# Optimization experiments

Hardware: AMD Instinct MI355X
Metric: run time of the kernel (lower is better)

Reference implementation:

```python
import jax, jax.numpy as jnp
import numpy as np

PROPAGATION_RANGE = 2
PROP_OUT = PROPAGATION_RANGE - 1  # propagation_out_range


def setup_inputs() -> dict:
    key = jax.random.key(0)
    k1, k2 = jax.random.split(key)
    B, D, H, W = 2, 48, 512, 640
    neighbors = 9
    depth_min = jnp.full((B,), 425.0, dtype=jnp.float32)
    depth_max = jnp.full((B,), 935.0, dtype=jnp.float32)
    # depth samples uniformly inside [depth_min, depth_max]
    u = jax.random.uniform(k1, (B, D, H, W), dtype=jnp.float32)
    depth_sample = depth_min[:, None, None, None] + u * (depth_max - depth_min)[:, None, None, None]
    # per-neighbor weights (2*neighbors channels: far-range then near-range)
    offset = jax.random.uniform(k2, (B, 2 * neighbors, H, W), dtype=jnp.float32) / neighbors
    return {
        "depth_sample": depth_sample,
        "depth_min": depth_min,
        "depth_max": depth_max,
        "offset": offset,
        "patchmatch_interval_scale": 0.025,
        "evaluate_neighbors": neighbors,
    }


def reference(depth_sample, depth_min, depth_max, offset, patchmatch_interval_scale, evaluate_neighbors):
    neighbors = int(evaluate_neighbors)
    B, D, H, W = depth_sample.shape
    k = int(np.sqrt(neighbors))  # square neighborhood side

    # normalized inverse depth in [0, 1]
    inv_min = 1.0 / depth_min  # [B]
    inv_max = 1.0 / depth_max  # [B]
    x = (1.0 / depth_sample - inv_max[:, None, None, None]) / (inv_min - inv_max)[:, None, None, None]

    pad = k // 2 + PROP_OUT
    pad1 = 2 * pad
    xp = jnp.pad(x, ((0, 0), (0, 0), (pad, pad), (pad, pad)), mode="reflect")
    xp1 = jnp.pad(x, ((0, 0), (0, 0), (pad1, pad1), (pad1, pad1)), mode="reflect")

    step = PROP_OUT + 1
    acc = jnp.zeros_like(x)
    for s in range(neighbors):  # small static loop (9 neighbors)
        iy, ix = (s // k) * step, (s % k) * step
        iy1, ix1 = 2 * iy, 2 * ix
        # offset channel broadcasts over the depth dimension
        f1 = offset[:, s, None] * xp1[:, :, iy1:H + iy1, ix1:W + ix1]
        f = offset[:, s + neighbors, None] * xp[:, :, iy:H + iy, ix:W + ix]
        acc = acc + (f + f1) * 0.5

    x1 = jnp.abs(acc - x) / patchmatch_interval_scale
    x1 = jnp.clip(x1, 0.0, 4.0)
    return jax.nn.sigmoid((2.0 - x1) * 2.0)
```

## Files before the change

### kernel.cpp

```cpp
#include <hip/hip_runtime.h>

constexpr int Bc = 2, Dc = 48, Hc = 512, Wc = 640;
constexpr int HWc = Hc * Wc;

constexpr int TW = 64, TH = 16, NT = 256;
constexpr int HALO = 4;
constexpr int SW = TW + 2 * HALO;
constexpr int SH = TH + 2 * HALO;
constexpr int PLANE = SW * SH;
constexpr int DC = 2;
constexpr int DSPLIT = 2;
constexpr int DCHUNK = Dc / DSPLIT;
constexpr int NIT = DCHUNK / DC;
constexpr int NVEC = DC * PLANE / 4;
constexpr int VPT = (NVEC + NT - 1) / NT;
constexpr int NSC = DC * PLANE;
constexpr int SPT = (NSC + NT - 1) / NT;

__device__ __forceinline__ int reflect_h(int h) {
    return h < 0 ? -h : (h >= Hc ? 2 * (Hc - 1) - h : h);
}
__device__ __forceinline__ int reflect_w(int w) {
    return w < 0 ? -w : (w >= Wc ? 2 * (Wc - 1) - w : w);
}

__global__ __launch_bounds__(NT) void dw_kernel(
    const float* __restrict__ ds, const float* __restrict__ dmin,
    const float* __restrict__ dmax, const float* __restrict__ off,
    const float* __restrict__ scale_p, float* __restrict__ out)
{
    __shared__ float sx[2][DC * PLANE];

    const int bz   = blockIdx.z;
    const int b    = bz >> 1;
    const int dch  = bz & 1;
    const int h0   = blockIdx.y * TH;
    const int w0   = blockIdx.x * TW;
    const int tid  = threadIdx.x;
    const int col4 = tid & 15;
    const int row  = tid >> 4;

    const float inv_min   = 1.0f / dmin[b];
    const float inv_max   = 1.0f / dmax[b];
    const float invd      = 1.0f / (inv_min - inv_max);
    const float inv_scale = 1.0f / scale_p[0];

    float offF[9][4], offN[9][4];
    {
        const float* op = off + (size_t)b * 18 * HWc
                        + (size_t)(h0 + row) * Wc + (w0 + 4 * col4);
        #pragma unroll
        for (int s = 0; s < 9; ++s) {
            float4 vF = *(const float4*)(op + (size_t)s * HWc);
            float4 vN = *(const float4*)(op + (size_t)(s + 9) * HWc);
            offF[s][0] = vF.x; offF[s][1] = vF.y; offF[s][2] = vF.z; offF[s][3] = vF.w;
            offN[s][0] = vN.x; offN[s][1] = vN.y; offN[s][2] = vN.z; offN[s][3] = vN.w;
        }
    }

    const float* dsb  = ds  + ((size_t)b * Dc + dch * DCHUNK) * HWc;
    float*       outb = out + (size_t)b * Dc * HWc
                            + (size_t)(h0 + row) * Wc + (w0 + 4 * col4);
    const int dg0 = dch * DCHUNK;

    auto compute = [&](const float* sb, int dglob0) {
        #pragma unroll
        for (int p = 0; p < DC; ++p) {
            const float* base = sb + p * PLANE + (row + HALO) * SW + 4 * col4;
            float acc[4] = {0.f, 0.f, 0.f, 0.f};
            float x0[4], rb[12];
            auto ld12 = [&](const float* q) {
                *(float4*)(rb)     = *(const float4*)(q);
                *(float4*)(rb + 4) = *(const float4*)(q + 4);
                *(float4*)(rb + 8) = *(const float4*)(q + 8);
            };
            ld12(base - 4 * SW);
            #pragma unroll
            for (int j = 0; j < 4; ++j)
                acc[j] += offF[0][j]*rb[j] + offF[1][j]*rb[j+4] + offF[2][j]*rb[j+8];
            ld12(base - 2 * SW);
            #pragma unroll
            for (int j = 0; j < 4; ++j)
                acc[j] += offN[0][j]*rb[j+2] + offN[1][j]*rb[j+4] + offN[2][j]*rb[j+6];
            ld12(base);
            #pragma unroll
            for (int j = 0; j < 4; ++j) {
                x0[j] = rb[j + 4];
                acc[j] += offN[3][j]*rb[j+2] + offN[4][j]*rb[j+4] + offN[5][j]*rb[j+6]
                        + offF[3][j]*rb[j]   + offF[4][j]*rb[j+4] + offF[5][j]*rb[j+8];
            }
            ld12(base + 2 * SW);
            #pragma unroll
            for (int j = 0; j < 4; ++j)
                acc[j] += offN[6][j]*rb[j+2] + offN[7][j]*rb[j+4] + offN[8][j]*rb[j+6];
            ld12(base + 4 * SW);
            #pragma unroll
            for (int j = 0; j < 4; ++j)
                acc[j] += offF[6][j]*rb[j] + offF[7][j]*rb[j+4] + offF[8][j]*rb[j+8];

            float4 o; float* po = (float*)&o;
            #pragma unroll
            for (int j = 0; j < 4; ++j) {
                float a  = 0.5f * acc[j];
                float x1 = fminf(fabsf(a - x0[j]) * inv_scale, 4.0f);
                float t  = 4.0f - 2.0f * x1;
                po[j] = __builtin_amdgcn_rcpf(1.0f + __expf(-t));
            }
            *(float4*)(outb + (size_t)(dglob0 + p) * HWc) = o;
        }
    };

    const bool interior = (blockIdx.x > 0) && (blockIdx.x + 1 < gridDim.x);

    if (interior) {
        int vsrc[VPT];
        #pragma unroll
        for (int i = 0; i < VPT; ++i) {
            int vid = tid + i * NT;
            if (vid < NVEC) {
                int p   = vid / (PLANE / 4);
                int rem = vid - p * (PLANE / 4);
                int r   = rem / (SW / 4);
                int j   = rem - r * (SW / 4);
                int hs  = reflect_h(h0 + r - HALO);
                vsrc[i] = p * HWc + hs * Wc + (w0 - HALO + 4 * j);
            } else vsrc[i] = 0;
        }
        float4 pre[VPT];
        auto issue = [&](int d0) {
            const float* dp = dsb + (size_t)d0 * HWc;
            #pragma unroll
            for (int i = 0; i < VPT; ++i) {
                int vid = tid + i * NT;
                if (vid < NVEC) pre[i] = *(const float4*)(dp + vsrc[i]);
            }
        };
        auto commit = [&](float* sb) {
            #pragma unroll
            for (int i = 0; i < VPT; ++i) {
                int vid = tid + i * NT;
                if (vid < NVEC) {
                    float4 v = pre[i], x;
                    x.x = (__builtin_amdgcn_rcpf(v.x) - inv_max) * invd;
                    x.y = (__builtin_amdgcn_rcpf(v.y) - inv_max) * invd;
                    x.z = (__builtin_amdgcn_rcpf(v.z) - inv_max) * invd;
                    x.w = (__builtin_amdgcn_rcpf(v.w) - inv_max) * invd;
                    *(float4*)(sb + vid * 4) = x;
                }
            }
        };
        issue(0);
        commit(sx[0]);
        __syncthreads();
        for (int it = 0; it < NIT; ++it) {
            if (it + 1 < NIT) issue((it + 1) * DC);
            compute(sx[it & 1], dg0 + it * DC);
            if (it + 1 < NIT) commit(sx[(it + 1) & 1]);
            __syncthreads();
        }
    } else {
        int ssrc[SPT];
        #pragma unroll
        for (int i = 0; i < SPT; ++i) {
            int idx = tid + i * NT;
            if (idx < NSC) {
                int p   = idx / PLANE;
                int rem = idx - p * PLANE;
                int r   = rem / SW;
                int c   = rem - r * SW;
                int hs  = reflect_h(h0 + r - HALO);
                int ws  = reflect_w(w0 + c - HALO);
                ssrc[i] = p * HWc + hs * Wc + ws;
            } else ssrc[i] = 0;
        }
        float pre[SPT];
        auto issue = [&](int d0) {
            const float* dp = dsb + (size_t)d0 * HWc;
            #pragma unroll
            for (int i = 0; i < SPT; ++i) {
                int idx = tid + i * NT;
                if (idx < NSC) pre[i] = dp[ssrc[i]];
            }
        };
        auto commit = [&](float* sb) {
            #pragma unroll
            for (int i = 0; i < SPT; ++i) {
                int idx = tid + i * NT;
                if (idx < NSC)
                    sb[idx] = (__builtin_amdgcn_rcpf(pre[i]) - inv_max) * invd;
            }
        };
        issue(0);
        commit(sx[0]);
        __syncthreads();
        for (int it = 0; it < NIT; ++it) {
            if (it + 1 < NIT) issue((it + 1) * DC);
            compute(sx[it & 1], dg0 + it * DC);
            if (it + 1 < NIT) commit(sx[(it + 1) & 1]);
            __syncthreads();
        }
    }
}

extern "C" void kernel_launch(void* const* d_in, const int* in_sizes, int n_in,
                              void* d_out, int out_size, void* d_ws, size_t ws_size,
                              hipStream_t stream) {
    const float* ds   = (const float*)d_in[0];
    const float* dmin = (const float*)d_in[1];
    const float* dmax = (const float*)d_in[2];
    const float* off  = (const float*)d_in[3];
    const float* sc   = (const float*)d_in[4];
    float* out = (float*)d_out;

    dim3 grid(Wc / TW, Hc / TH, Bc * DSPLIT);
    dw_kernel<<<grid, NT, 0, stream>>>(ds, dmin, dmax, off, sc, out);
}
```

Measured before the change: 270.4 us.

## Narrow tiles to 32 columns, 2 pixels per thread, drop depth split

Halves the tile width so each thread computes two adjacent pixels with float2 shared-memory loads instead of four with float4. The depth dimension is no longer split across blocks; each block loops over all 48 depths, with twice as many blocks along width. This cuts per-thread register use for the offset weights (36 instead of 72), which may raise occupancy. The cost is a larger halo overhead relative to the tile (40/32 instead of 72/64), so more redundant global loads and reciprocals per output.

```diff
diff --git a/kernel.cpp b/kernel.cpp
--- a/kernel.cpp
+++ b/kernel.cpp
@@ -3,15 +3,13 @@
 constexpr int Bc = 2, Dc = 48, Hc = 512, Wc = 640;
 constexpr int HWc = Hc * Wc;
 
-constexpr int TW = 64, TH = 16, NT = 256;
+constexpr int TW = 32, TH = 16, NT = 256;
 constexpr int HALO = 4;
 constexpr int SW = TW + 2 * HALO;
 constexpr int SH = TH + 2 * HALO;
 constexpr int PLANE = SW * SH;
 constexpr int DC = 2;
-constexpr int DSPLIT = 2;
-constexpr int DCHUNK = Dc / DSPLIT;
-constexpr int NIT = DCHUNK / DC;
+constexpr int NIT = Dc / DC;
 constexpr int NVEC = DC * PLANE / 4;
 constexpr int VPT = (NVEC + NT - 1) / NT;
 constexpr int NSC = DC * PLANE;
@@ -31,82 +29,78 @@
 {
     __shared__ float sx[2][DC * PLANE];
 
-    const int bz   = blockIdx.z;
-    const int b    = bz >> 1;
-    const int dch  = bz & 1;
-    const int h0   = blockIdx.y * TH;
-    const int w0   = blockIdx.x * TW;
-    const int tid  = threadIdx.x;
-    const int col4 = tid & 15;
-    const int row  = tid >> 4;
+    const int b   = blockIdx.z;
+    const int h0  = blockIdx.y * TH;
+    const int w0  = blockIdx.x * TW;
+    const int tid = threadIdx.x;
+    const int col = tid & 15;
+    const int row = tid >> 4;
 
     const float inv_min   = 1.0f / dmin[b];
     const float inv_max   = 1.0f / dmax[b];
     const float invd      = 1.0f / (inv_min - inv_max);
     const float inv_scale = 1.0f / scale_p[0];
 
-    float offF[9][4], offN[9][4];
+    float offF[9][2], offN[9][2];
     {
         const float* op = off + (size_t)b * 18 * HWc
-                        + (size_t)(h0 + row) * Wc + (w0 + 4 * col4);
+                        + (size_t)(h0 + row) * Wc + (w0 + 2 * col);
         #pragma unroll
         for (int s = 0; s < 9; ++s) {
-            float4 vF = *(const float4*)(op + (size_t)s * HWc);
-            float4 vN = *(const float4*)(op + (size_t)(s + 9) * HWc);
-            offF[s][0] = vF.x; offF[s][1] = vF.y; offF[s][2] = vF.z; offF[s][3] = vF.w;
-            offN[s][0] = vN.x; offN[s][1] = vN.y; offN[s][2] = vN.z; offN[s][3] = vN.w;
+            float2 vF = *(const float2*)(op + (size_t)s * HWc);
+            float2 vN = *(const float2*)(op + (size_t)(s + 9) * HWc);
+            offF[s][0] = vF.x; offF[s][1] = vF.y;
+            offN[s][0] = vN.x; offN[s][1] = vN.y;
         }
     }
 
-    const float* dsb  = ds  + ((size_t)b * Dc + dch * DCHUNK) * HWc;
+    const float* dsb  = ds  + (size_t)b * Dc * HWc;
     float*       outb = out + (size_t)b * Dc * HWc
-                            + (size_t)(h0 + row) * Wc + (w0 + 4 * col4);
-    const int dg0 = dch * DCHUNK;
-
-    auto compute = [&](const float* sb, int dglob0) {
+                            + (size_t)(h0 + row) * Wc + (w0 + 2 * col);
+
+    auto compute = [&](const float* sb, int d0) {
         #pragma unroll
         for (int p = 0; p < DC; ++p) {
-            const float* base = sb + p * PLANE + (row + HALO) * SW + 4 * col4;
-            float acc[4] = {0.f, 0.f, 0.f, 0.f};
-            float x0[4], rb[12];
-            auto ld12 = [&](const float* q) {
-                *(float4*)(rb)     = *(const float4*)(q);
-                *(float4*)(rb + 4) = *(const float4*)(q + 4);
-                *(float4*)(rb + 8) = *(const float4*)(q + 8);
-            };
-            ld12(base - 4 * SW);
-            #pragma unroll
-            for (int j = 0; j < 4; ++j)
-                acc[j] += offF[0][j]*rb[j] + offF[1][j]*rb[j+4] + offF[2][j]*rb[j+8];
-            ld12(base - 2 * SW);
-            #pragma unroll
-            for (int j = 0; j < 4; ++j)
-                acc[j] += offN[0][j]*rb[j+2] + offN[1][j]*rb[j+4] + offN[2][j]*rb[j+6];
-            ld12(base);
-            #pragma unroll
-            for (int j = 0; j < 4; ++j) {
-                x0[j] = rb[j + 4];
-                acc[j] += offN[3][j]*rb[j+2] + offN[4][j]*rb[j+4] + offN[5][j]*rb[j+6]
-                        + offF[3][j]*rb[j]   + offF[4][j]*rb[j+4] + offF[5][j]*rb[j+8];
-            }
-            ld12(base + 2 * SW);
-            #pragma unroll
-            for (int j = 0; j < 4; ++j)
-                acc[j] += offN[6][j]*rb[j+2] + offN[7][j]*rb[j+4] + offN[8][j]*rb[j+6];
-            ld12(base + 4 * SW);
-            #pragma unroll
-            for (int j = 0; j < 4; ++j)
-                acc[j] += offF[6][j]*rb[j] + offF[7][j]*rb[j+4] + offF[8][j]*rb[j+8];
-
-            float4 o; float* po = (float*)&o;
-            #pragma unroll
-            for (int j = 0; j < 4; ++j) {
-                float a  = 0.5f * acc[j];
-                float x1 = fminf(fabsf(a - x0[j]) * inv_scale, 4.0f);
-                float t  = 4.0f - 2.0f * x1;
-                po[j] = __builtin_amdgcn_rcpf(1.0f + __expf(-t));
-            }
-            *(float4*)(outb + (size_t)(dglob0 + p) * HWc) = o;
+            const float* bp = sb + p * PLANE + (row + HALO) * SW + (HALO + 2 * col);
+            float a0 = 0.f, a1 = 0.f, x00, x01;
+            float2 t0, t1, t2, t3, t4;
+            t0 = *(const float2*)(bp - 4 * SW - 4);
+            t1 = *(const float2*)(bp - 4 * SW);
+            t2 = *(const float2*)(bp - 4 * SW + 4);
+            a0 += offF[0][0]*t0.x + offF[1][0]*t1.x + offF[2][0]*t2.x;
+            a1 += offF[0][1]*t0.y + offF[1][1]*t1.y + offF[2][1]*t2.y;
+            t0 = *(const float2*)(bp - 2 * SW - 2);
+            t1 = *(const float2*)(bp - 2 * SW);
+            t2 = *(const float2*)(bp - 2 * SW + 2);
+            a0 += offN[0][0]*t0.x + offN[1][0]*t1.x + offN[2][0]*t2.x;
+            a1 += offN[0][1]*t0.y + offN[1][1]*t1.y + offN[2][1]*t2.y;
+            t0 = *(const float2*)(bp - 4);
+            t1 = *(const float2*)(bp - 2);
+            t2 = *(const float2*)(bp);
+            t3 = *(const float2*)(bp + 2);
+            t4 = *(const float2*)(bp + 4);
+            x00 = t2.x; x01 = t2.y;
+            a0 += offN[3][0]*t1.x + offN[4][0]*t2.x + offN[5][0]*t3.x
+                + offF[3][0]*t0.x + offF[4][0]*t2.x + offF[5][0]*t4.x;
+            a1 += offN[3][1]*t1.y + offN[4][1]*t2.y + offN[5][1]*t3.y
+                + offF[3][1]*t0.y + offF[4][1]*t2.y + offF[5][1]*t4.y;
+            t0 = *(const float2*)(bp + 2 * SW - 2);
+            t1 = *(const float2*)(bp + 2 * SW);
+            t2 = *(const float2*)(bp + 2 * SW + 2);
+            a0 += offN[6][0]*t0.x + offN[7][0]*t1.x + offN[8][0]*t2.x;
+            a1 += offN[6][1]*t0.y + offN[7][1]*t1.y + offN[8][1]*t2.y;
+            t0 = *(const float2*)(bp + 4 * SW - 4);
+            t1 = *(const float2*)(bp + 4 * SW);
+            t2 = *(const float2*)(bp + 4 * SW + 4);
+            a0 += offF[6][0]*t0.x + offF[7][0]*t1.x + offF[8][0]*t2.x;
+            a1 += offF[6][1]*t0.y + offF[7][1]*t1.y + offF[8][1]*t2.y;
+            float2 o;
+            a0 *= 0.5f; a1 *= 0.5f;
+            float x1a = fminf(fabsf(a0 - x00) * inv_scale, 4.0f);
+            float x1b = fminf(fabsf(a1 - x01) * inv_scale, 4.0f);
+            o.x = __builtin_amdgcn_rcpf(1.0f + __expf(-(4.0f - 2.0f * x1a)));
+            o.y = __builtin_amdgcn_rcpf(1.0f + __expf(-(4.0f - 2.0f * x1b)));
+            *(float2*)(outb + (size_t)(d0 + p) * HWc) = o;
         }
     };
 
@@ -154,7 +148,7 @@
         __syncthreads();
         for (int it = 0; it < NIT; ++it) {
             if (it + 1 < NIT) issue((it + 1) * DC);
-            compute(sx[it & 1], dg0 + it * DC);
+            compute(sx[it & 1], it * DC);
             if (it + 1 < NIT) commit(sx[(it + 1) & 1]);
             __syncthreads();
         }
@@ -195,7 +189,7 @@
         __syncthreads();
         for (int it = 0; it < NIT; ++it) {
             if (it + 1 < NIT) issue((it + 1) * DC);
-            compute(sx[it & 1], dg0 + it * DC);
+            compute(sx[it & 1], it * DC);
             if (it + 1 < NIT) commit(sx[(it + 1) & 1]);
             __syncthreads();
         }
@@ -212,6 +206,6 @@
     const float* sc   = (const float*)d_in[4];
     float* out = (float*)d_out;
 
-    dim3 grid(Wc / TW, Hc / TH, Bc * DSPLIT);
+    dim3 grid(Wc / TW, Hc / TH, Bc);
     dw_kernel<<<grid, NT, 0, stream>>>(ds, dmin, dmax, off, sc, out);
 }
```

Result: slower. 279.3 us (+3.3%).
